# Performance work log

Measured on AMD Instinct MI355X. Metric: run time of the kernel, lower is better.

Reference implementation:

```python
import jax, jax.numpy as jnp
import numpy as np

NU, NI, D, C, V, E, L = 100000, 50000, 128, 5, 200000, 200000, 10


def setup_inputs() -> dict:
    key = jax.random.key(0)
    ks = jax.random.split(key, 16)
    s = lambda fan_in: 1.0 / np.sqrt(fan_in)
    return {
        "urf": jax.random.normal(ks[0], (NU, D), jnp.float32),
        "irf": jax.random.normal(ks[1], (NI, D), jnp.float32),
        "utf": jax.random.normal(ks[2], (NU, D), jnp.float32),
        "itf": jax.random.normal(ks[3], (NI, D), jnp.float32),
        "w1r": jax.random.normal(ks[4], (2 * D, D), jnp.float32) * s(2 * D),
        "w2r": jax.random.normal(ks[5], (D, D), jnp.float32) * s(D),
        "w1t": jax.random.normal(ks[6], (2 * D, D), jnp.float32) * s(2 * D),
        "w2t": jax.random.normal(ks[7], (D, D), jnp.float32) * s(D),
        "wp": jax.random.normal(ks[8], (D, C), jnp.float32) * s(D),
        "emb": jax.random.normal(ks[9], (V, D), jnp.float32),
        "src": jax.random.randint(ks[10], (E,), 0, NU, jnp.int32),
        "dst": jax.random.randint(ks[11], (E,), 0, NI, jnp.int32),
        "sentence_id": jax.random.randint(ks[12], (E, L), 0, V, jnp.int32),
        "neg_sid": jax.random.randint(ks[13], (E, L), 1, V, jnp.int32),
    }


def _review_feature(emb, sid):
    # masked mean-pool of sentence embeddings: [E, L] -> [E, D]
    length = (sid > 0).astype(jnp.float32).sum(axis=-1, keepdims=True) + 1e-9
    return emb[sid].sum(axis=-2) / length


def reference(urf, irf, utf, itf, w1r, w2r, w1t, w2t, wp, emb,
              src, dst, sentence_id, neg_sid):
    # edge-wise gather of src (user) / dst (item) features + concat  [E, 2D]
    rf = jnp.concatenate([urf[src], irf[dst]], axis=1)
    rh = jax.nn.relu(rf @ w1r) @ w2r                      # rating_linear  [E, D]
    pr = rh @ wp                                          # rating_predictor [E, C]
    tf = jnp.concatenate([utf[src], itf[dst]], axis=1)
    th = jax.nn.relu(tf @ w1t) @ w2t + rh                 # topic_linear + residual
    pos_review = _review_feature(emb, sentence_id)        # [E, D]
    neg_review = _review_feature(emb, neg_sid)            # [E, D]
    pos_score = (th * pos_review).sum(axis=1)             # [E]
    neg_score = (th * neg_review).sum(axis=1)
    loss = -jax.nn.log_sigmoid(pos_score - neg_score)     # -log(sigmoid(pos-neg))
    return pr, loss.mean(), loss.mean()
```

## Files before the change

kernel.cpp:

```cpp
#include <hip/hip_runtime.h>

#define NU_ 100000
#define NI_ 50000
#define D_  128
#define C_  5
#define V_  200000
#define E_  200000
#define L_  10

typedef __bf16 bf16x8 __attribute__((ext_vector_type(8)));
typedef unsigned short u16;
typedef u16 u16x8 __attribute__((ext_vector_type(8)));
typedef float f32x4 __attribute__((ext_vector_type(4)));

#define W1R_OFF 0
#define W2R_OFF 32768
#define W1T_OFF 49152
#define W2T_OFF 81920
#define WTOT    98304

__device__ __forceinline__ u16 f2bf(float x) {
    union { float f; unsigned int u; } v; v.f = x;
    unsigned int u = v.u;
    return (u16)((u + 0x7FFFu + ((u >> 16) & 1u)) >> 16);
}

__global__ void prep_kernel(const float* __restrict__ w1r, const float* __restrict__ w2r,
                            const float* __restrict__ w1t, const float* __restrict__ w2t,
                            u16* __restrict__ wbuf, float* __restrict__ loss_acc) {
    int idx = blockIdx.x * blockDim.x + threadIdx.x;
    if (idx == 0) *loss_acc = 0.f;
    if (idx >= WTOT) return;
    const float* src; int base;
    if (idx < W2R_OFF)      { src = w1r; base = W1R_OFF; }
    else if (idx < W1T_OFF) { src = w2r; base = W2R_OFF; }
    else if (idx < W2T_OFF) { src = w1t; base = W1T_OFF; }
    else                    { src = w2t; base = W2T_OFF; }
    int local = idx - base;
    int j = local & 7;
    int g = local >> 3;
    int n = g & 127;
    int kq = g >> 7;
    wbuf[idx] = f2bf(src[(kq * 8 + j) * 128 + n]);
}

__device__ __forceinline__ void stage_half(const float* __restrict__ row, int lane, u16* buf) {
    int m = lane >> 2, q = lane & 3;
    const float* seg = row + q * 32;
#pragma unroll
    for (int i = 0; i < 4; i++) {
        float4 a = *(const float4*)(seg + i * 8);
        float4 b = *(const float4*)(seg + i * 8 + 4);
        u16x8 v;
        v[0] = f2bf(a.x); v[1] = f2bf(a.y); v[2] = f2bf(a.z); v[3] = f2bf(a.w);
        v[4] = f2bf(b.x); v[5] = f2bf(b.y); v[6] = f2bf(b.z); v[7] = f2bf(b.w);
        *(u16x8*)(buf + ((q * 4 + i) * 16 + m) * 8) = v;
    }
}

template <int KT>
__device__ __forceinline__ void gemm_tile(const u16* aLDS, const u16* __restrict__ Wg,
                                          int lq, int ln, f32x4 acc[8]) {
#pragma unroll
    for (int kt = 0; kt < KT; kt++) {
        bf16x8 af = *(const bf16x8*)(aLDS + ((kt * 4 + lq) * 16 + ln) * 8);
#pragma unroll
        for (int nt = 0; nt < 8; nt++) {
            bf16x8 bfv = *(const bf16x8*)(Wg + (size_t)((kt * 4 + lq) * 128 + nt * 16 + ln) * 8);
            acc[nt] = __builtin_amdgcn_mfma_f32_16x16x32_bf16(af, bfv, acc[nt], 0, 0, 0);
        }
    }
}

__device__ __forceinline__ void store_h_relu(const f32x4 acc[8], u16* buf, int lq, int ln) {
#pragma unroll
    for (int nt = 0; nt < 8; nt++)
#pragma unroll
        for (int reg = 0; reg < 4; reg++) {
            float h = fmaxf(acc[nt][reg], 0.f);
            int dcol = nt * 16 + ln;
            int r = lq * 4 + reg;
            buf[((dcol >> 3) * 16 + r) * 8 + (dcol & 7)] = f2bf(h);
        }
}

__device__ __forceinline__ void mlp(const float* __restrict__ uF, const float* __restrict__ iF,
                                    const int* __restrict__ srcI, const int* __restrict__ dstI,
                                    int ebase, int lane, int lq, int ln,
                                    const u16* __restrict__ w1, const u16* __restrict__ w2,
                                    u16* bufA, u16* bufB, f32x4 acc[8]) {
    int e = ebase + (lane >> 2);
    int su = srcI[e], sd = dstI[e];
    f32x4 h1[8];
#pragma unroll
    for (int nt = 0; nt < 8; nt++) h1[nt] = (f32x4){0.f, 0.f, 0.f, 0.f};

    stage_half(uF + (size_t)su * D_, lane, bufA);
    __syncthreads();
    gemm_tile<4>(bufA, w1, lq, ln, h1);
    __syncthreads();
    stage_half(iF + (size_t)sd * D_, lane, bufA);
    __syncthreads();
    gemm_tile<4>(bufA, w1 + 16384, lq, ln, h1);
    store_h_relu(h1, bufB, lq, ln);
    __syncthreads();
    gemm_tile<4>(bufB, w2, lq, ln, acc);
}

__device__ __forceinline__ float softplus_(float x) {
    return fmaxf(x, 0.f) + log1pf(expf(-fabsf(x)));
}

__global__ __launch_bounds__(256, 3) void fused_kernel(
    const float* __restrict__ urf, const float* __restrict__ irf,
    const float* __restrict__ utf, const float* __restrict__ itf,
    const float* __restrict__ wp, const float* __restrict__ emb,
    const int* __restrict__ srcI, const int* __restrict__ dstI,
    const int* __restrict__ sidI, const int* __restrict__ nsidI,
    const u16* __restrict__ wbuf, float* __restrict__ loss_acc,
    float* __restrict__ out) {
    __shared__ u16 smem[4 * 4096];
    const int tid = threadIdx.x;
    const int w = tid >> 6;
    const int lane = tid & 63;
    const int lq = lane >> 4;
    const int ln = lane & 15;
    u16* bufA = smem + w * 4096;
    u16* bufB = bufA + 2048;
    const int ebase = blockIdx.x * 64 + w * 16;

    f32x4 rh[8];
#pragma unroll
    for (int nt = 0; nt < 8; nt++) rh[nt] = (f32x4){0.f, 0.f, 0.f, 0.f};
    mlp(urf, irf, srcI, dstI, ebase, lane, lq, ln,
        wbuf + W1R_OFF, wbuf + W2R_OFF, bufA, bufB, rh);

    {
        float pp[4][5];
#pragma unroll
        for (int r = 0; r < 4; r++)
#pragma unroll
            for (int c = 0; c < 5; c++) pp[r][c] = 0.f;
#pragma unroll
        for (int nt = 0; nt < 8; nt++) {
            int d = nt * 16 + ln;
            float wpc[5];
#pragma unroll
            for (int c = 0; c < 5; c++) wpc[c] = wp[d * 5 + c];
#pragma unroll
            for (int reg = 0; reg < 4; reg++)
#pragma unroll
                for (int c = 0; c < 5; c++) pp[reg][c] += rh[nt][reg] * wpc[c];
        }
#pragma unroll
        for (int off = 1; off < 16; off <<= 1)
#pragma unroll
            for (int reg = 0; reg < 4; reg++)
#pragma unroll
                for (int c = 0; c < 5; c++)
                    pp[reg][c] += __shfl_xor(pp[reg][c], off, 64);
        if (ln == 0) {
#pragma unroll
            for (int reg = 0; reg < 4; reg++) {
                int e = ebase + lq * 4 + reg;
#pragma unroll
                for (int c = 0; c < 5; c++) out[(size_t)e * 5 + c] = pp[reg][c];
            }
        }
    }

    __syncthreads();
    f32x4 th[8];
#pragma unroll
    for (int nt = 0; nt < 8; nt++) th[nt] = rh[nt];
    mlp(utf, itf, srcI, dstI, ebase, lane, lq, ln,
        wbuf + W1T_OFF, wbuf + W2T_OFF, bufA, bufB, th);

    __syncthreads();
    float* thb = (float*)bufA;
#pragma unroll
    for (int nt = 0; nt < 8; nt++)
#pragma unroll
        for (int reg = 0; reg < 4; reg++)
            thb[(lq * 4 + reg) * 128 + nt * 16 + ln] = th[nt][reg];
    __syncthreads();

    float wave_loss = 0.f;
    const int h = lane >> 5, hl = lane & 31;
    for (int mp = 0; mp < 16; mp += 2) {
        int m = mp + h;
        int e = ebase + m;
        float4 t4 = *(const float4*)(thb + m * 128 + hl * 4);
        const int* sp = sidI + e * L_;
        const int* np = nsidI + e * L_;
        float ps = 0.f, ns = 0.f;
        int pcnt = 0, ncnt = 0;
#pragma unroll
        for (int i = 0; i < L_; i++) {
            int s = sp[i];
            pcnt += (s > 0) ? 1 : 0;
            float4 ev = *(const float4*)(emb + (size_t)s * D_ + hl * 4);
            ps += t4.x * ev.x + t4.y * ev.y + t4.z * ev.z + t4.w * ev.w;
        }
#pragma unroll
        for (int i = 0; i < L_; i++) {
            int s = np[i];
            ncnt += (s > 0) ? 1 : 0;
            float4 ev = *(const float4*)(emb + (size_t)s * D_ + hl * 4);
            ns += t4.x * ev.x + t4.y * ev.y + t4.z * ev.z + t4.w * ev.w;
        }
#pragma unroll
        for (int off = 1; off < 32; off <<= 1) {
            ps += __shfl_xor(ps, off, 64);
            ns += __shfl_xor(ns, off, 64);
        }
        if (hl == 0) {
            ps /= ((float)pcnt + 1e-9f);
            ns /= ((float)ncnt + 1e-9f);
            wave_loss += softplus_(ns - ps);
        }
    }
    wave_loss += __shfl_xor(wave_loss, 32, 64);
    if (lane == 0) atomicAdd(loss_acc, wave_loss);
}

__global__ void finish_kernel(const float* __restrict__ loss_acc, float* __restrict__ out) {
    float v = loss_acc[0] * (1.0f / (float)E_);
    out[(size_t)E_ * C_]     = v;
    out[(size_t)E_ * C_ + 1] = v;
}

extern "C" void kernel_launch(void* const* d_in, const int* in_sizes, int n_in,
                              void* d_out, int out_size, void* d_ws, size_t ws_size,
                              hipStream_t stream) {
    const float* urf = (const float*)d_in[0];
    const float* irf = (const float*)d_in[1];
    const float* utf = (const float*)d_in[2];
    const float* itf = (const float*)d_in[3];
    const float* w1r = (const float*)d_in[4];
    const float* w2r = (const float*)d_in[5];
    const float* w1t = (const float*)d_in[6];
    const float* w2t = (const float*)d_in[7];
    const float* wp  = (const float*)d_in[8];
    const float* emb = (const float*)d_in[9];
    const int* srcI  = (const int*)d_in[10];
    const int* dstI  = (const int*)d_in[11];
    const int* sidI  = (const int*)d_in[12];
    const int* nsidI = (const int*)d_in[13];
    float* out = (float*)d_out;

    float* loss_acc = (float*)d_ws;
    u16* wbuf = (u16*)((char*)d_ws + 256);

    prep_kernel<<<(WTOT + 255) / 256, 256, 0, stream>>>(w1r, w2r, w1t, w2t, wbuf, loss_acc);
    fused_kernel<<<E_ / 64, 256, 0, stream>>>(urf, irf, utf, itf, wp, emb,
                                              srcI, dstI, sidI, nsidI,
                                              wbuf, loss_acc, out);
    finish_kernel<<<1, 1, 0, stream>>>(loss_acc, out);
}
```

Measured before the change: 647.7 us.

## Convert embedding table to bf16 in workspace and gather bf16 rows

Adds a per-call kernel that converts the 200000x128 fp32 embedding table to bf16 in workspace, then has the review-scoring stage gather 16-byte bf16 chunks (8 elements per lane, 16 lanes per edge) instead of fp32 float4 chunks. This halves the bytes pulled by the random gathers of 20 embedding rows per edge. In exchange the conversion pass reads the full 102 MB table and writes 51 MB every call, and the dot products lose precision. It falls back to the fp32 path when the workspace is too small.

```diff
diff --git a/kernel.cpp b/kernel.cpp
--- a/kernel.cpp
+++ b/kernel.cpp
@@ -18,11 +18,19 @@
 #define W1T_OFF 49152
 #define W2T_OFF 81920
 #define WTOT    98304
+#define EMB_BYTE_OFF (256 * 1024)
+#define EMB_ELEMS    (V_ * D_)
 
 __device__ __forceinline__ u16 f2bf(float x) {
     union { float f; unsigned int u; } v; v.f = x;
     unsigned int u = v.u;
     return (u16)((u + 0x7FFFu + ((u >> 16) & 1u)) >> 16);
+}
+__device__ __forceinline__ float bfhi(unsigned int u) {
+    union { unsigned int u; float f; } v; v.u = u & 0xFFFF0000u; return v.f;
+}
+__device__ __forceinline__ float bflo(unsigned int u) {
+    union { unsigned int u; float f; } v; v.u = u << 16; return v.f;
 }
 
 __global__ void prep_kernel(const float* __restrict__ w1r, const float* __restrict__ w2r,
@@ -44,6 +52,17 @@
     wbuf[idx] = f2bf(src[(kq * 8 + j) * 128 + n]);
 }
 
+__global__ void cvt_kernel(const float* __restrict__ src, u16* __restrict__ dst, int n8) {
+    int i = blockIdx.x * blockDim.x + threadIdx.x;
+    if (i >= n8) return;
+    float4 a = *(const float4*)(src + (size_t)i * 8);
+    float4 b = *(const float4*)(src + (size_t)i * 8 + 4);
+    u16x8 v;
+    v[0] = f2bf(a.x); v[1] = f2bf(a.y); v[2] = f2bf(a.z); v[3] = f2bf(a.w);
+    v[4] = f2bf(b.x); v[5] = f2bf(b.y); v[6] = f2bf(b.z); v[7] = f2bf(b.w);
+    *(u16x8*)(dst + (size_t)i * 8) = v;
+}
+
 __device__ __forceinline__ void stage_half(const float* __restrict__ row, int lane, u16* buf) {
     int m = lane >> 2, q = lane & 3;
     const float* seg = row + q * 32;
@@ -111,10 +130,12 @@
     return fmaxf(x, 0.f) + log1pf(expf(-fabsf(x)));
 }
 
+template <bool EB>
 __global__ __launch_bounds__(256, 3) void fused_kernel(
     const float* __restrict__ urf, const float* __restrict__ irf,
     const float* __restrict__ utf, const float* __restrict__ itf,
     const float* __restrict__ wp, const float* __restrict__ emb,
+    const u16* __restrict__ embB,
     const int* __restrict__ srcI, const int* __restrict__ dstI,
     const int* __restrict__ sidI, const int* __restrict__ nsidI,
     const u16* __restrict__ wbuf, float* __restrict__ loss_acc,
@@ -178,49 +199,106 @@
 
     __syncthreads();
     float* thb = (float*)bufA;
-#pragma unroll
-    for (int nt = 0; nt < 8; nt++)
-#pragma unroll
-        for (int reg = 0; reg < 4; reg++)
-            thb[(lq * 4 + reg) * 128 + nt * 16 + ln] = th[nt][reg];
+    if constexpr (EB) {
+#pragma unroll
+        for (int nt = 0; nt < 8; nt++)
+#pragma unroll
+            for (int reg = 0; reg < 4; reg++) {
+                int col = nt * 16 + ln;
+                thb[((lq * 4 + reg) * 16 + (col >> 3)) * 8 + (col & 7)] = th[nt][reg];
+            }
+    } else {
+#pragma unroll
+        for (int nt = 0; nt < 8; nt++)
+#pragma unroll
+            for (int reg = 0; reg < 4; reg++)
+                thb[(lq * 4 + reg) * 128 + nt * 16 + ln] = th[nt][reg];
+    }
     __syncthreads();
 
     float wave_loss = 0.f;
-    const int h = lane >> 5, hl = lane & 31;
-    for (int mp = 0; mp < 16; mp += 2) {
-        int m = mp + h;
-        int e = ebase + m;
-        float4 t4 = *(const float4*)(thb + m * 128 + hl * 4);
-        const int* sp = sidI + e * L_;
-        const int* np = nsidI + e * L_;
-        float ps = 0.f, ns = 0.f;
-        int pcnt = 0, ncnt = 0;
-#pragma unroll
-        for (int i = 0; i < L_; i++) {
-            int s = sp[i];
-            pcnt += (s > 0) ? 1 : 0;
-            float4 ev = *(const float4*)(emb + (size_t)s * D_ + hl * 4);
-            ps += t4.x * ev.x + t4.y * ev.y + t4.z * ev.z + t4.w * ev.w;
-        }
-#pragma unroll
-        for (int i = 0; i < L_; i++) {
-            int s = np[i];
-            ncnt += (s > 0) ? 1 : 0;
-            float4 ev = *(const float4*)(emb + (size_t)s * D_ + hl * 4);
-            ns += t4.x * ev.x + t4.y * ev.y + t4.z * ev.z + t4.w * ev.w;
-        }
-#pragma unroll
-        for (int off = 1; off < 32; off <<= 1) {
-            ps += __shfl_xor(ps, off, 64);
-            ns += __shfl_xor(ns, off, 64);
-        }
-        if (hl == 0) {
-            ps /= ((float)pcnt + 1e-9f);
-            ns /= ((float)ncnt + 1e-9f);
-            wave_loss += softplus_(ns - ps);
-        }
-    }
-    wave_loss += __shfl_xor(wave_loss, 32, 64);
+    if constexpr (EB) {
+        const int g = lane >> 4, gl = lane & 15;
+        for (int it = 0; it < 4; it++) {
+            int m = it * 4 + g;
+            int e = ebase + m;
+            float th8[8];
+            *(f32x4*)th8       = *(const f32x4*)(thb + (m * 16 + gl) * 8);
+            *(f32x4*)(th8 + 4) = *(const f32x4*)(thb + (m * 16 + gl) * 8 + 4);
+            float ps = 0.f, ns = 0.f;
+            int pcnt = 0, ncnt = 0;
+#pragma unroll
+            for (int i = 0; i < L_; i++) {
+                int s = sidI[e * L_ + i];
+                pcnt += (s > 0) ? 1 : 0;
+                union { u16x8 v; unsigned int u[4]; } cv;
+                cv.v = *(const u16x8*)(embB + (size_t)s * D_ + gl * 8);
+#pragma unroll
+                for (int k = 0; k < 4; k++) {
+                    ps = fmaf(th8[2 * k],     bflo(cv.u[k]), ps);
+                    ps = fmaf(th8[2 * k + 1], bfhi(cv.u[k]), ps);
+                }
+            }
+#pragma unroll
+            for (int i = 0; i < L_; i++) {
+                int s = nsidI[e * L_ + i];
+                ncnt += (s > 0) ? 1 : 0;
+                union { u16x8 v; unsigned int u[4]; } cv;
+                cv.v = *(const u16x8*)(embB + (size_t)s * D_ + gl * 8);
+#pragma unroll
+                for (int k = 0; k < 4; k++) {
+                    ns = fmaf(th8[2 * k],     bflo(cv.u[k]), ns);
+                    ns = fmaf(th8[2 * k + 1], bfhi(cv.u[k]), ns);
+                }
+            }
+#pragma unroll
+            for (int off = 1; off < 16; off <<= 1) {
+                ps += __shfl_xor(ps, off, 64);
+                ns += __shfl_xor(ns, off, 64);
+            }
+            if (gl == 0) {
+                ps /= ((float)pcnt + 1e-9f);
+                ns /= ((float)ncnt + 1e-9f);
+                wave_loss += softplus_(ns - ps);
+            }
+        }
+        wave_loss += __shfl_xor(wave_loss, 16, 64);
+        wave_loss += __shfl_xor(wave_loss, 32, 64);
+    } else {
+        const int h = lane >> 5, hl = lane & 31;
+        for (int mp = 0; mp < 16; mp += 2) {
+            int m = mp + h;
+            int e = ebase + m;
+            float4 t4 = *(const float4*)(thb + m * 128 + hl * 4);
+            float ps = 0.f, ns = 0.f;
+            int pcnt = 0, ncnt = 0;
+#pragma unroll
+            for (int i = 0; i < L_; i++) {
+                int s = sidI[e * L_ + i];
+                pcnt += (s > 0) ? 1 : 0;
+                float4 ev = *(const float4*)(emb + (size_t)s * D_ + hl * 4);
+                ps += t4.x * ev.x + t4.y * ev.y + t4.z * ev.z + t4.w * ev.w;
+            }
+#pragma unroll
+            for (int i = 0; i < L_; i++) {
+                int s = nsidI[e * L_ + i];
+                ncnt += (s > 0) ? 1 : 0;
+                float4 ev = *(const float4*)(emb + (size_t)s * D_ + hl * 4);
+                ns += t4.x * ev.x + t4.y * ev.y + t4.z * ev.z + t4.w * ev.w;
+            }
+#pragma unroll
+            for (int off = 1; off < 32; off <<= 1) {
+                ps += __shfl_xor(ps, off, 64);
+                ns += __shfl_xor(ns, off, 64);
+            }
+            if (hl == 0) {
+                ps /= ((float)pcnt + 1e-9f);
+                ns /= ((float)ncnt + 1e-9f);
+                wave_loss += softplus_(ns - ps);
+            }
+        }
+        wave_loss += __shfl_xor(wave_loss, 32, 64);
+    }
     if (lane == 0) atomicAdd(loss_acc, wave_loss);
 }
 
@@ -251,10 +329,22 @@
 
     float* loss_acc = (float*)d_ws;
     u16* wbuf = (u16*)((char*)d_ws + 256);
+    u16* embB = (u16*)((char*)d_ws + EMB_BYTE_OFF);
+
+    bool eb = ws_size >= (size_t)EMB_BYTE_OFF + (size_t)EMB_ELEMS * 2;
 
     prep_kernel<<<(WTOT + 255) / 256, 256, 0, stream>>>(w1r, w2r, w1t, w2t, wbuf, loss_acc);
-    fused_kernel<<<E_ / 64, 256, 0, stream>>>(urf, irf, utf, itf, wp, emb,
-                                              srcI, dstI, sidI, nsidI,
-                                              wbuf, loss_acc, out);
+    if (eb)
+        cvt_kernel<<<(EMB_ELEMS / 8 + 255) / 256, 256, 0, stream>>>(emb, embB, EMB_ELEMS / 8);
+
+    if (eb)
+        fused_kernel<true><<<E_ / 64, 256, 0, stream>>>(
+            urf, irf, utf, itf, wp, emb, embB,
+            srcI, dstI, sidI, nsidI, wbuf, loss_acc, out);
+    else
+        fused_kernel<false><<<E_ / 64, 256, 0, stream>>>(
+            urf, irf, utf, itf, wp, emb, embB,
+            srcI, dstI, sidI, nsidI, wbuf, loss_acc, out);
+
     finish_kernel<<<1, 1, 0, stream>>>(loss_acc, out);
 }
```

Result: faster. 588.7 us (-9.1%).
